# Optimization experiments

Measured on AMD Instinct MI355X. Metric: run time of the kernel, lower is better.

Reference implementation:

```python
import jax, jax.numpy as jnp
import numpy as np

B, S, D, H = 4, 1024, 1024, 16
DK = D // H
EPS = 1e-6

def setup_inputs() -> dict:
    key = jax.random.key(0)
    ks = jax.random.split(key, 7)
    scale = 1.0 / np.sqrt(D)
    return {
        "query": jax.random.normal(ks[0], (B, S, D), jnp.float32),
        "key": jax.random.normal(ks[1], (B, S, D), jnp.float32),
        "value": jax.random.normal(ks[2], (B, S, D), jnp.float32),
        "Wq": jax.random.normal(ks[3], (D, D), jnp.float32) * scale,
        "Wk": jax.random.normal(ks[4], (D, D), jnp.float32) * scale,
        "Wv": jax.random.normal(ks[5], (D, D), jnp.float32) * scale,
        "Wo": jax.random.normal(ks[6], (D, D), jnp.float32) * scale,
        "ln_gamma": jnp.ones((D,), jnp.float32),
        "ln_beta": jnp.zeros((D,), jnp.float32),
    }

def reference(query, key, value, Wq, Wk, Wv, Wo, ln_gamma, ln_beta):
    residual = query
    # projections (torch Linear: x @ W.T); reshape to [B,H,S,DK]
    def proj(x, W):
        y = jnp.einsum('bsd,ed->bse', x, W)
        return y.reshape(B, S, H, DK).transpose(0, 2, 1, 3)
    q, k, v = proj(query, Wq), proj(key, Wk), proj(value, Wv)
    scores = jnp.einsum('bhqd,bhkd->bhqk', q, k) / jnp.sqrt(jnp.float32(DK))
    p = jax.nn.softmax(scores, axis=-1)
    x = jnp.einsum('bhqk,bhkd->bhqd', p, v)
    x = x.transpose(0, 2, 1, 3).reshape(B, S, D)
    x = jnp.einsum('bsd,ed->bse', x, Wo)
    x = x + residual
    mu = jnp.mean(x, axis=-1, keepdims=True)
    var = jnp.var(x, axis=-1, keepdims=True)
    x = (x - mu) / jnp.sqrt(var + EPS) * ln_gamma + ln_beta
    return x
```

## Files before the change

kernel.cpp:

```cpp
#include <hip/hip_runtime.h>
#include <hip/hip_bf16.h>

#define B_ 4
#define S_ 1024
#define D_ 1024
#define H_ 16
#define DK_ 64
#define MROWS (B_*S_)

typedef short bf16x8 __attribute__((ext_vector_type(8)));
typedef float f32x4 __attribute__((ext_vector_type(4)));
typedef unsigned short u16;
typedef unsigned u32;
typedef u16 u16x4 __attribute__((ext_vector_type(4)));

__device__ __forceinline__ u16 f2bf(float f) {
    union { float f; unsigned u; } v; v.f = f;
    unsigned u = v.u;
    u += 0x7fff + ((u >> 16) & 1);
    return (u16)(u >> 16);
}

__device__ __forceinline__ void gld_lds16(const u16* gp, u16* lp) {
    __builtin_amdgcn_global_load_lds(
        (const __attribute__((address_space(1))) void*)gp,
        (__attribute__((address_space(3))) void*)lp,
        16, 0, 0);
}

__global__ __launch_bounds__(256) void pack_w(
    const float* __restrict__ wq, const float* __restrict__ wk,
    const float* __restrict__ wv, const float* __restrict__ wo,
    u16* __restrict__ w_dst)
{
    const int NW = 4 * D_ * D_;
    for (int c = blockIdx.x * blockDim.x + threadIdx.x;
         c < NW / 4; c += gridDim.x * blockDim.x) {
        int e = c * 4;
        int t = e >> 20;
        int off = e & (1048576 - 1);
        const float* s = (t == 0 ? wq : t == 1 ? wk : t == 2 ? wv : wo) + off;
        float4 tv = *(const float4*)s;
        u16x4 o; o[0]=f2bf(tv.x); o[1]=f2bf(tv.y); o[2]=f2bf(tv.z); o[3]=f2bf(tv.w);
        *(u16x4*)(w_dst + e) = o;
    }
}

__global__ __launch_bounds__(256) void gemm_qkv(
    const float* __restrict__ Aq, const float* __restrict__ Ak,
    const float* __restrict__ Avv, const u16* __restrict__ Wb,
    u16* __restrict__ Cb)
{
    __shared__ u16 ldsA[128 * 64];
    __shared__ u16 ldsB[128 * 64];

    const int gx = gridDim.x, gy = gridDim.y, gz = gridDim.z;
    const int nwg = gx * gy * gz;
    const int flat = blockIdx.x + gx * (blockIdx.y + gy * blockIdx.z);
    const int f = (flat & 7) * (nwg >> 3) + (flat >> 3);
    const int bx = f % gx;
    const int rem = f / gx;
    const int by = rem % gy;
    const int z = rem / gy;

    const float* Af = (z == 0) ? Aq : (z == 1) ? Ak : Avv;
    Wb += (size_t)z * D_ * D_;

    const int tid = threadIdx.x, lane = tid & 63, wid = tid >> 6;
    const int wr = wid >> 1, wc = wid & 1;
    const int m0 = by * 128, n0 = bx * 128;
    const int wbase = wid * 64;

    f32x4 acc[4][4] = {};

    for (int kt = 0; kt < 1024; kt += 64) {
        __syncthreads();
        #pragma unroll
        for (int j = 0; j < 4; ++j) {
            int g2 = j * 256 + tid;
            int row = g2 >> 3, c8 = g2 & 7;
            const float* src = Af + (size_t)(m0 + row) * 1024 + kt + c8 * 8;
            float4 a0 = *(const float4*)(src);
            float4 a1 = *(const float4*)(src + 4);
            bf16x8 o;
            o[0] = (short)f2bf(a0.x); o[1] = (short)f2bf(a0.y);
            o[2] = (short)f2bf(a0.z); o[3] = (short)f2bf(a0.w);
            o[4] = (short)f2bf(a1.x); o[5] = (short)f2bf(a1.y);
            o[6] = (short)f2bf(a1.z); o[7] = (short)f2bf(a1.w);
            int c8s = c8 ^ (row & 7);
            *(bf16x8*)(&ldsA[row * 64 + c8s * 8]) = o;
        }
        #pragma unroll
        for (int j = 0; j < 4; ++j) {
            int ch = j * 256 + tid;
            int row = ch >> 3, c8 = (ch & 7) ^ (row & 7);
            gld_lds16(Wb + (size_t)(n0 + row) * 1024 + kt + c8 * 8,
                      &ldsB[(j * 256 + wbase) * 8]);
        }
        __syncthreads();

        #pragma unroll
        for (int ks = 0; ks < 2; ++ks) {
            const int cb = ks * 32 + (lane >> 4) * 8;
            bf16x8 af[4], bfr[4];
            #pragma unroll
            for (int m = 0; m < 4; ++m) {
                int row = wr * 64 + m * 16 + (lane & 15);
                af[m] = *(const bf16x8*)(&ldsA[row * 64 + (cb ^ ((row & 7) << 3))]);
            }
            #pragma unroll
            for (int n = 0; n < 4; ++n) {
                int row = wc * 64 + n * 16 + (lane & 15);
                bfr[n] = *(const bf16x8*)(&ldsB[row * 64 + (cb ^ ((row & 7) << 3))]);
            }
            #pragma unroll
            for (int m = 0; m < 4; ++m)
                #pragma unroll
                for (int n = 0; n < 4; ++n)
                    acc[m][n] = __builtin_amdgcn_mfma_f32_16x16x32_bf16(
                        af[m], bfr[n], acc[m][n], 0, 0, 0);
        }
    }

    if (z == 2) {
        u16* Cz = Cb + 2 * (size_t)MROWS * D_;
        #pragma unroll
        for (int m = 0; m < 4; ++m)
            #pragma unroll
            for (int n = 0; n < 4; ++n) {
                u16x4 o;
                #pragma unroll
                for (int r = 0; r < 4; ++r) o[r] = f2bf(acc[m][n][r]);
                int grow = m0 + wr * 64 + m * 16 + (lane >> 4) * 4;
                int gcol = n0 + wc * 64 + n * 16 + (lane & 15);
                *(u16x4*)(&Cz[(size_t)gcol * MROWS + grow]) = o;
            }
    } else {
        u16* Cz = Cb + (size_t)z * MROWS * D_;
        #pragma unroll
        for (int m = 0; m < 4; ++m)
            #pragma unroll
            for (int n = 0; n < 4; ++n)
                #pragma unroll
                for (int r = 0; r < 4; ++r) {
                    int grow = m0 + wr * 64 + m * 16 + (lane >> 4) * 4 + r;
                    int gcol = n0 + wc * 64 + n * 16 + (lane & 15);
                    Cz[(size_t)grow * 1024 + gcol] = f2bf(acc[m][n][r]);
                }
    }
}

template<int BM, bool EPI_RESID, bool VT>
__global__ __launch_bounds__(256) void gemm_fast(
    const u16* __restrict__ Ab, const u16* __restrict__ Wb,
    u16* __restrict__ Cb, float* __restrict__ Cf, const float* __restrict__ resid)
{
    constexpr int WN = (BM == 128) ? 2 : 4;
    constexpr int WCOLS = 128 / WN;
    constexpr int NR = WCOLS / 16;
    __shared__ u16 ldsA[BM * 64];
    __shared__ u16 ldsB[128 * 64];

    const int gx = gridDim.x, gy = gridDim.y, gz = gridDim.z;
    const int nwg = gx * gy * gz;
    const int flat = blockIdx.x + gx * (blockIdx.y + gy * blockIdx.z);
    const int f = (flat & 7) * (nwg >> 3) + (flat >> 3);
    const int bx = f % gx;
    const int rem = f / gx;
    const int by = rem % gy;
    const int z = rem / gy;

    Ab += (size_t)z * MROWS * D_;
    Wb += (size_t)z * D_ * D_;
    const u16* CbT = Cb + (EPI_RESID ? 0 : (size_t)z * MROWS * D_);
    u16* Cbz = (u16*)CbT;

    const int tid = threadIdx.x, lane = tid & 63, wid = tid >> 6;
    const int wr = (BM == 128) ? (wid >> 1) : 0;
    const int wc = (BM == 128) ? (wid & 1) : wid;
    const int m0 = by * BM, n0 = bx * 128;
    const int wbase = wid * 64;

    f32x4 acc[4][NR] = {};

    for (int kt = 0; kt < 1024; kt += 64) {
        __syncthreads();
        #pragma unroll
        for (int j = 0; j < BM / 32; ++j) {
            int ch = j * 256 + tid;
            int row = ch >> 3, c8 = (ch & 7) ^ (row & 7);
            gld_lds16(Ab + (size_t)(m0 + row) * 1024 + kt + c8 * 8,
                      &ldsA[(j * 256 + wbase) * 8]);
        }
        #pragma unroll
        for (int j = 0; j < 4; ++j) {
            int ch = j * 256 + tid;
            int row = ch >> 3, c8 = (ch & 7) ^ (row & 7);
            gld_lds16(Wb + (size_t)(n0 + row) * 1024 + kt + c8 * 8,
                      &ldsB[(j * 256 + wbase) * 8]);
        }
        __syncthreads();

        #pragma unroll
        for (int ks = 0; ks < 2; ++ks) {
            const int cb = ks * 32 + (lane >> 4) * 8;
            bf16x8 af[4], bfr[NR];
            #pragma unroll
            for (int m = 0; m < 4; ++m) {
                int row = wr * 64 + m * 16 + (lane & 15);
                af[m] = *(const bf16x8*)(&ldsA[row * 64 + (cb ^ ((row & 7) << 3))]);
            }
            #pragma unroll
            for (int n = 0; n < NR; ++n) {
                int row = wc * WCOLS + n * 16 + (lane & 15);
                bfr[n] = *(const bf16x8*)(&ldsB[row * 64 + (cb ^ ((row & 7) << 3))]);
            }
            #pragma unroll
            for (int m = 0; m < 4; ++m)
                #pragma unroll
                for (int n = 0; n < NR; ++n)
                    acc[m][n] = __builtin_amdgcn_mfma_f32_16x16x32_bf16(
                        af[m], bfr[n], acc[m][n], 0, 0, 0);
        }
    }

    if (VT && z == 2) {
        #pragma unroll
        for (int m = 0; m < 4; ++m)
            #pragma unroll
            for (int n = 0; n < NR; ++n) {
                u16x4 o;
                #pragma unroll
                for (int r = 0; r < 4; ++r) o[r] = f2bf(acc[m][n][r]);
                int grow = m0 + wr * 64 + m * 16 + (lane >> 4) * 4;
                int gcol = n0 + wc * WCOLS + n * 16 + (lane & 15);
                *(u16x4*)(&Cbz[(size_t)gcol * MROWS + grow]) = o;
            }
    } else {
        #pragma unroll
        for (int m = 0; m < 4; ++m)
            #pragma unroll
            for (int n = 0; n < NR; ++n)
                #pragma unroll
                for (int r = 0; r < 4; ++r) {
                    int grow = m0 + wr * 64 + m * 16 + (lane >> 4) * 4 + r;
                    int gcol = n0 + wc * WCOLS + n * 16 + (lane & 15);
                    if (EPI_RESID)
                        Cf[(size_t)grow * 1024 + gcol] = acc[m][n][r] + resid[(size_t)grow * 1024 + gcol];
                    else
                        Cbz[(size_t)grow * 1024 + gcol] = f2bf(acc[m][n][r]);
                }
    }
}

template<bool A_BF16, bool EPI_RESID>
__global__ __launch_bounds__(256) void gemm_bt(
    const void* __restrict__ Av, const float* __restrict__ Bw,
    u16* __restrict__ Cb, float* __restrict__ Cf,
    const float* __restrict__ resid, int M, int N, int K)
{
    __shared__ u16 lds[2][128 * 64];
    const int tid  = threadIdx.x;
    const int lane = tid & 63;
    const int wid  = tid >> 6;
    const int wr = wid >> 1, wc = wid & 1;
    const int m0 = blockIdx.y * 128, n0 = blockIdx.x * 128;

    f32x4 acc[4][4] = {};

    for (int kt = 0; kt < K; kt += 64) {
        #pragma unroll
        for (int j = 0; j < 8; ++j) {
            int idx4 = tid + 256 * j;
            int r = idx4 >> 4;
            int c = (idx4 & 15) * 4;
            u16x4 aw, bw;
            if (A_BF16) {
                const u16* Ab2 = (const u16*)Av;
                aw = *(const u16x4*)(Ab2 + (size_t)(m0 + r) * K + kt + c);
            } else {
                const float* Af = (const float*)Av;
                float4 t = *(const float4*)(Af + (size_t)(m0 + r) * K + kt + c);
                aw[0] = f2bf(t.x); aw[1] = f2bf(t.y); aw[2] = f2bf(t.z); aw[3] = f2bf(t.w);
            }
            {
                float4 t = *(const float4*)(Bw + (size_t)(n0 + r) * K + kt + c);
                bw[0] = f2bf(t.x); bw[1] = f2bf(t.y); bw[2] = f2bf(t.z); bw[3] = f2bf(t.w);
            }
            int sa = r * 64 + (c ^ ((r & 7) << 3));
            *(u16x4*)(&lds[0][sa]) = aw;
            *(u16x4*)(&lds[1][sa]) = bw;
        }
        __syncthreads();
        #pragma unroll
        for (int ks = 0; ks < 2; ++ks) {
            const int cb = ks * 32 + (lane >> 4) * 8;
            bf16x8 af[4], bfr[4];
            #pragma unroll
            for (int m = 0; m < 4; ++m) {
                int row = wr * 64 + m * 16 + (lane & 15);
                af[m] = *(const bf16x8*)(&lds[0][row * 64 + (cb ^ ((row & 7) << 3))]);
            }
            #pragma unroll
            for (int n = 0; n < 4; ++n) {
                int row = wc * 64 + n * 16 + (lane & 15);
                bfr[n] = *(const bf16x8*)(&lds[1][row * 64 + (cb ^ ((row & 7) << 3))]);
            }
            #pragma unroll
            for (int m = 0; m < 4; ++m)
                #pragma unroll
                for (int n = 0; n < 4; ++n)
                    acc[m][n] = __builtin_amdgcn_mfma_f32_16x16x32_bf16(
                        af[m], bfr[n], acc[m][n], 0, 0, 0);
        }
        __syncthreads();
    }

    #pragma unroll
    for (int m = 0; m < 4; ++m)
        #pragma unroll
        for (int n = 0; n < 4; ++n)
            #pragma unroll
            for (int r = 0; r < 4; ++r) {
                int grow = m0 + wr * 64 + m * 16 + (lane >> 4) * 4 + r;
                int gcol = n0 + wc * 64 + n * 16 + (lane & 15);
                float v = acc[m][n][r];
                if (EPI_RESID)
                    Cf[(size_t)grow * N + gcol] = v + resid[(size_t)grow * N + gcol];
                else
                    Cb[(size_t)grow * N + gcol] = f2bf(v);
            }
}

__global__ __launch_bounds__(512, 4) void attn_fwd5(
    const u16* __restrict__ Qg, const u16* __restrict__ Kg,
    const u16* __restrict__ Vt, u16* __restrict__ Og)
{
    __shared__ u16 qs[128 * 64];
    __shared__ u16 ks2[64 * 64];
    __shared__ u16 vsT[64 * 64];
    __shared__ u16 ps[128 * 64];

    const int tid = threadIdx.x, lane = tid & 63, w = tid >> 6;
    const int g = lane >> 4, ql = lane & 15;

    const int bid = blockIdx.x;
    const int f = (bid & 7) * 64 + (bid >> 3);
    const int qt = f & 7, h = (f >> 3) & 15, b = f >> 7;
    const int q0 = qt * 128;
    const size_t rbase = (size_t)b * S_;
    const int cb0 = h * DK_;

    auto stage_kv = [&](int kv0) {
        {
            int ch = tid;
            int row = ch >> 3, c8 = (ch & 7) ^ (row & 7);
            gld_lds16(Kg + (rbase + kv0 + row) * D_ + cb0 + c8 * 8, &ks2[w * 512]);
        }
        {
            int ch = tid;
            int row = ch >> 3, c8 = (ch & 7) ^ (row & 7);
            gld_lds16(Vt + (size_t)(cb0 + row) * MROWS + rbase + kv0 + c8 * 8, &vsT[w * 512]);
        }
    };

    #pragma unroll
    for (int j = 0; j < 2; ++j) {
        int idx = j * 512 + tid;
        int row = idx >> 3, c8 = (idx & 7) ^ (row & 7);
        gld_lds16(Qg + (rbase + q0 + row) * D_ + cb0 + c8 * 8,
                  &qs[(j * 512 + w * 64) * 8]);
    }
    stage_kv(0);
    __syncthreads();

    bf16x8 qb[2];
    {
        const int q = w * 16 + ql;
        #pragma unroll
        for (int ks = 0; ks < 2; ++ks) {
            int c = 32 * ks + 8 * g;
            qb[ks] = *(const bf16x8*)(&qs[q * 64 + (c ^ ((q & 7) << 3))]);
        }
    }

    float mrow = -1e30f, lrow = 0.f;
    f32x4 xacc[4] = {};

    for (int jt = 0; jt < 16; ++jt) {
        f32x4 sacc[4] = {};
        __builtin_amdgcn_s_setprio(1);
        #pragma unroll
        for (int ks = 0; ks < 2; ++ks) {
            #pragma unroll
            for (int n = 0; n < 4; ++n) {
                int krow = n * 16 + ql;
                int c = 32 * ks + 8 * g;
                bf16x8 kf = *(const bf16x8*)(&ks2[krow * 64 + (c ^ ((krow & 7) << 3))]);
                sacc[n] = __builtin_amdgcn_mfma_f32_16x16x32_bf16(kf, qb[ks], sacc[n], 0, 0, 0);
            }
        }
        __builtin_amdgcn_s_setprio(0);

        float mt = sacc[0][0];
        #pragma unroll
        for (int n = 0; n < 4; ++n)
            #pragma unroll
            for (int r = 0; r < 4; ++r) mt = fmaxf(mt, sacc[n][r]);
        mt = fmaxf(mt, __shfl_xor(mt, 16));
        mt = fmaxf(mt, __shfl_xor(mt, 32));
        float mnew = fmaxf(mrow, mt * 0.125f);
        float alpha = __expf(mrow - mnew);
        float rsum = 0.f;
        u16 pb[16];
        #pragma unroll
        for (int n = 0; n < 4; ++n)
            #pragma unroll
            for (int r = 0; r < 4; ++r) {
                float p = __expf(sacc[n][r] * 0.125f - mnew);
                rsum += p;
                pb[n * 4 + r] = f2bf(p);
            }
        rsum += __shfl_xor(rsum, 16);
        rsum += __shfl_xor(rsum, 32);
        lrow = lrow * alpha + rsum;
        mrow = mnew;

        {
            const int q = w * 16 + ql;
            #pragma unroll
            for (int n = 0; n < 4; ++n) {
                int c = 16 * n + 4 * g;
                *(u16x4*)(&ps[q * 64 + (c ^ ((q & 7) << 3))]) = *(const u16x4*)(&pb[n * 4]);
            }
        }
        asm volatile("s_waitcnt lgkmcnt(0)" ::: "memory");
        __builtin_amdgcn_sched_barrier(0);

        bf16x8 pa[2];
        {
            const int q = w * 16 + ql;
            #pragma unroll
            for (int ks = 0; ks < 2; ++ks) {
                int c = 32 * ks + 8 * g;
                pa[ks] = *(const bf16x8*)(&ps[q * 64 + (c ^ ((q & 7) << 3))]);
            }
        }
        #pragma unroll
        for (int r = 0; r < 4; ++r) {
            float a_r = __shfl(alpha, 4 * g + r);
            #pragma unroll
            for (int n2 = 0; n2 < 4; ++n2) xacc[n2][r] *= a_r;
        }

        __builtin_amdgcn_s_setprio(1);
        #pragma unroll
        for (int ks = 0; ks < 2; ++ks)
            #pragma unroll
            for (int n2 = 0; n2 < 4; ++n2) {
                int vrow = n2 * 16 + ql;
                int c2 = 32 * ks + 8 * g;
                bf16x8 bv = *(const bf16x8*)(&vsT[vrow * 64 + (c2 ^ ((vrow & 7) << 3))]);
                xacc[n2] = __builtin_amdgcn_mfma_f32_16x16x32_bf16(pa[ks], bv, xacc[n2], 0, 0, 0);
            }
        __builtin_amdgcn_s_setprio(0);

        if (jt < 15) {
            __syncthreads();
            stage_kv((jt + 1) * 64);
            __syncthreads();
        }
    }

    float linv[4];
    #pragma unroll
    for (int r = 0; r < 4; ++r) linv[r] = 1.f / __shfl(lrow, 4 * g + r);
    #pragma unroll
    for (int n2 = 0; n2 < 4; ++n2)
        #pragma unroll
        for (int r = 0; r < 4; ++r) {
            int qrow = q0 + w * 16 + 4 * g + r;
            int col = cb0 + n2 * 16 + ql;
            Og[(rbase + qrow) * D_ + col] = f2bf(xacc[n2][r] * linv[r]);
        }
}

__global__ __launch_bounds__(256) void attn_fwd(
    const u16* __restrict__ Qg, const u16* __restrict__ Kg,
    const u16* __restrict__ Vg, u16* __restrict__ Og)
{
    __shared__ u16 qs[64 * 64], ks2[64 * 64], vt[64 * 64], ps[64 * 64];
    const int tid = threadIdx.x, lane = tid & 63, w = tid >> 6;
    const int b = blockIdx.z, h = blockIdx.y, q0 = blockIdx.x * 64;
    const size_t rbase = (size_t)b * S_;
    const int cb0 = h * DK_;

    #pragma unroll
    for (int j = 0; j < 4; ++j) {
        int idx4 = tid + 256 * j;
        int r = idx4 >> 4, c = (idx4 & 15) * 4;
        u16x4 t = *(const u16x4*)(Qg + (rbase + q0 + r) * D_ + cb0 + c);
        *(u16x4*)(&qs[r * 64 + (c ^ ((r & 7) << 3))]) = t;
    }

    float mrow[4], lrow[4];
    f32x4 xacc[4] = {};
    #pragma unroll
    for (int r = 0; r < 4; ++r) { mrow[r] = -1e30f; lrow[r] = 0.f; }

    for (int jt = 0; jt < 16; ++jt) {
        const int kv0 = jt * 64;
        __syncthreads();
        #pragma unroll
        for (int j = 0; j < 4; ++j) {
            int idx4 = tid + 256 * j;
            int r = idx4 >> 4, c = (idx4 & 15) * 4;
            u16x4 t = *(const u16x4*)(Kg + (rbase + kv0 + r) * D_ + cb0 + c);
            *(u16x4*)(&ks2[r * 64 + (c ^ ((r & 7) << 3))]) = t;
            u16x4 tv = *(const u16x4*)(Vg + (rbase + kv0 + r) * D_ + cb0 + c);
            #pragma unroll
            for (int jj = 0; jj < 4; ++jj) {
                int d = c + jj;
                vt[d * 64 + (r ^ ((d & 7) << 3))] = tv[jj];
            }
        }
        __syncthreads();

        f32x4 sacc[4] = {};
        #pragma unroll
        for (int ks = 0; ks < 2; ++ks) {
            const int cb = ks * 32 + (lane >> 4) * 8;
            int qrow = w * 16 + (lane & 15);
            bf16x8 aq = *(const bf16x8*)(&qs[qrow * 64 + (cb ^ ((qrow & 7) << 3))]);
            #pragma unroll
            for (int n = 0; n < 4; ++n) {
                int krow = n * 16 + (lane & 15);
                bf16x8 bk = *(const bf16x8*)(&ks2[krow * 64 + (cb ^ ((krow & 7) << 3))]);
                sacc[n] = __builtin_amdgcn_mfma_f32_16x16x32_bf16(aq, bk, sacc[n], 0, 0, 0);
            }
        }

        #pragma unroll
        for (int r = 0; r < 4; ++r) {
            float mx = fmaxf(fmaxf(sacc[0][r], sacc[1][r]),
                             fmaxf(sacc[2][r], sacc[3][r]));
            mx = fmaxf(mx, __shfl_xor(mx, 1));
            mx = fmaxf(mx, __shfl_xor(mx, 2));
            mx = fmaxf(mx, __shfl_xor(mx, 4));
            mx = fmaxf(mx, __shfl_xor(mx, 8));
            float mnew = fmaxf(mrow[r], mx * 0.125f);
            float alpha = __expf(mrow[r] - mnew);
            float p[4], rsum = 0.f;
            #pragma unroll
            for (int n = 0; n < 4; ++n) { p[n] = __expf(sacc[n][r] * 0.125f - mnew); rsum += p[n]; }
            rsum += __shfl_xor(rsum, 1);
            rsum += __shfl_xor(rsum, 2);
            rsum += __shfl_xor(rsum, 4);
            rsum += __shfl_xor(rsum, 8);
            lrow[r] = lrow[r] * alpha + rsum;
            mrow[r] = mnew;
            int qrow = w * 16 + (lane >> 4) * 4 + r;
            #pragma unroll
            for (int n = 0; n < 4; ++n) {
                xacc[n][r] *= alpha;
                int col = n * 16 + (lane & 15);
                ps[qrow * 64 + (col ^ ((qrow & 7) << 3))] = f2bf(p[n]);
            }
        }
        __syncthreads();

        #pragma unroll
        for (int ks = 0; ks < 2; ++ks) {
            const int cb = ks * 32 + (lane >> 4) * 8;
            int prow = w * 16 + (lane & 15);
            bf16x8 ap = *(const bf16x8*)(&ps[prow * 64 + (cb ^ ((prow & 7) << 3))]);
            #pragma unroll
            for (int n = 0; n < 4; ++n) {
                int vrow = n * 16 + (lane & 15);
                bf16x8 bv = *(const bf16x8*)(&vt[vrow * 64 + (cb ^ ((vrow & 7) << 3))]);
                xacc[n] = __builtin_amdgcn_mfma_f32_16x16x32_bf16(ap, bv, xacc[n], 0, 0, 0);
            }
        }
    }

    #pragma unroll
    for (int n = 0; n < 4; ++n)
        #pragma unroll
        for (int r = 0; r < 4; ++r) {
            int qrow = q0 + w * 16 + (lane >> 4) * 4 + r;
            int col = cb0 + n * 16 + (lane & 15);
            Og[(rbase + qrow) * D_ + col] = f2bf(xacc[n][r] / lrow[r]);
        }
}

__global__ __launch_bounds__(256) void ln_inplace(
    float* __restrict__ Y, const float* __restrict__ g, const float* __restrict__ bt)
{
    __shared__ float red[2][4];
    const int row = blockIdx.x, tid = threadIdx.x;
    float4 v = *(const float4*)(Y + (size_t)row * D_ + tid * 4);
    float s = v.x + v.y + v.z + v.w;
    float q = v.x * v.x + v.y * v.y + v.z * v.z + v.w * v.w;
    #pragma unroll
    for (int m = 1; m < 64; m <<= 1) { s += __shfl_xor(s, m); q += __shfl_xor(q, m); }
    const int w = tid >> 6, lane = tid & 63;
    if (lane == 0) { red[0][w] = s; red[1][w] = q; }
    __syncthreads();
    s = red[0][0] + red[0][1] + red[0][2] + red[0][3];
    q = red[1][0] + red[1][1] + red[1][2] + red[1][3];
    float mu = s * (1.f / 1024.f);
    float var = q * (1.f / 1024.f) - mu * mu;
    float rstd = rsqrtf(var + 1e-6f);
    float4 gv = *(const float4*)(g + tid * 4);
    float4 bv = *(const float4*)(bt + tid * 4);
    v.x = (v.x - mu) * rstd * gv.x + bv.x;
    v.y = (v.y - mu) * rstd * gv.y + bv.y;
    v.z = (v.z - mu) * rstd * gv.z + bv.z;
    v.w = (v.w - mu) * rstd * gv.w + bv.w;
    *(float4*)(Y + (size_t)row * D_ + tid * 4) = v;
}

extern "C" void kernel_launch(void* const* d_in, const int* in_sizes, int n_in,
                              void* d_out, int out_size, void* d_ws, size_t ws_size,
                              hipStream_t stream)
{
    const float* query = (const float*)d_in[0];
    const float* key   = (const float*)d_in[1];
    const float* value = (const float*)d_in[2];
    const float* Wq    = (const float*)d_in[3];
    const float* Wk    = (const float*)d_in[4];
    const float* Wv    = (const float*)d_in[5];
    const float* Wo    = (const float*)d_in[6];
    const float* gamma = (const float*)d_in[7];
    const float* beta  = (const float*)d_in[8];
    float* out = (float*)d_out;

    const size_t ACT = (size_t)MROWS * D_;
    const size_t WSZ = (size_t)D_ * D_;
    const size_t NEED = (4 * WSZ + 4 * ACT) * 2;

    if (ws_size >= NEED) {
        u16* wb = (u16*)d_ws;
        u16* pb = wb + 4 * WSZ;
        u16* Ap = pb + 3 * ACT;

        pack_w<<<1024, 256, 0, stream>>>(Wq, Wk, Wv, Wo, wb);
        gemm_qkv<<<dim3(8, 32, 3), 256, 0, stream>>>(query, key, value, wb, pb);
        attn_fwd5<<<512, 512, 0, stream>>>(pb, pb + ACT, pb + 2 * ACT, Ap);
        gemm_fast<64, true, false><<<dim3(8, 64, 1), 256, 0, stream>>>(Ap, wb + 3 * WSZ, nullptr, out, query);
        ln_inplace<<<MROWS, 256, 0, stream>>>(out, gamma, beta);
    } else {
        u16* Qp = (u16*)d_ws;
        u16* Kp = Qp + ACT;
        u16* Vp = Kp + ACT;
        u16* Ap = Vp + ACT;
        dim3 gg(D_ / 128, MROWS / 128);
        gemm_bt<false, false><<<gg, 256, 0, stream>>>(query, Wq, Qp, nullptr, nullptr, MROWS, D_, D_);
        gemm_bt<false, false><<<gg, 256, 0, stream>>>(key,   Wk, Kp, nullptr, nullptr, MROWS, D_, D_);
        gemm_bt<false, false><<<gg, 256, 0, stream>>>(value, Wv, Vp, nullptr, nullptr, MROWS, D_, D_);
        attn_fwd<<<dim3(S_ / 64, H_, B_), 256, 0, stream>>>(Qp, Kp, Vp, Ap);
        gemm_bt<true, true><<<gg, 256, 0, stream>>>(Ap, Wo, nullptr, out, query, MROWS, D_, D_);
        ln_inplace<<<MROWS, 256, 0, stream>>>(out, gamma, beta);
    }
}
```

Baseline: 127.0 us.

## Pre-convert activations to bf16 and use 256x128 async-loaded QKV GEMM tiles

The fp32 query/key/value activations are now converted to bf16 in the packing kernel along with the weights. The QKV projection then loads both operands straight into LDS with global_load_lds, instead of doing fp32 loads and converting in registers inside the GEMM loop. The GEMM tile grows to 256x128 with 512 threads. This adds an extra pass that writes and rereads 24MB of bf16 activations, in exchange for a leaner GEMM inner loop and better operand reuse. The attention output buffer now aliases the activation staging area.

```diff
diff --git a/kernel.cpp b/kernel.cpp
--- a/kernel.cpp
+++ b/kernel.cpp
@@ -28,34 +28,45 @@
         16, 0, 0);
 }
 
-__global__ __launch_bounds__(256) void pack_w(
+__global__ __launch_bounds__(256) void pack_bf16(
+    const float* __restrict__ q, const float* __restrict__ k, const float* __restrict__ v,
     const float* __restrict__ wq, const float* __restrict__ wk,
     const float* __restrict__ wv, const float* __restrict__ wo,
-    u16* __restrict__ w_dst)
-{
-    const int NW = 4 * D_ * D_;
+    u16* __restrict__ act_dst, u16* __restrict__ w_dst)
+{
+    const int NACT = 3 * MROWS * D_;
+    const int NW   = 4 * D_ * D_;
     for (int c = blockIdx.x * blockDim.x + threadIdx.x;
-         c < NW / 4; c += gridDim.x * blockDim.x) {
+         c < (NACT + NW) / 4; c += gridDim.x * blockDim.x) {
         int e = c * 4;
-        int t = e >> 20;
-        int off = e & (1048576 - 1);
-        const float* s = (t == 0 ? wq : t == 1 ? wk : t == 2 ? wv : wo) + off;
+        const float* s; u16* d;
+        if (e < NACT) {
+            int t = e >> 22;
+            int off = e & (4194304 - 1);
+            s = (t == 0 ? q : t == 1 ? k : v) + off;
+            d = act_dst + e;
+        } else {
+            int e2 = e - NACT;
+            int t = e2 >> 20;
+            int off = e2 & (1048576 - 1);
+            s = (t == 0 ? wq : t == 1 ? wk : t == 2 ? wv : wo) + off;
+            d = w_dst + e2;
+        }
         float4 tv = *(const float4*)s;
         u16x4 o; o[0]=f2bf(tv.x); o[1]=f2bf(tv.y); o[2]=f2bf(tv.z); o[3]=f2bf(tv.w);
-        *(u16x4*)(w_dst + e) = o;
-    }
-}
-
-__global__ __launch_bounds__(256) void gemm_qkv(
-    const float* __restrict__ Aq, const float* __restrict__ Ak,
-    const float* __restrict__ Avv, const u16* __restrict__ Wb,
+        *(u16x4*)d = o;
+    }
+}
+
+__global__ __launch_bounds__(512) void gemm_qkv2(
+    const u16* __restrict__ Ab, const u16* __restrict__ Wb,
     u16* __restrict__ Cb)
 {
-    __shared__ u16 ldsA[128 * 64];
+    __shared__ u16 ldsA[256 * 64];
     __shared__ u16 ldsB[128 * 64];
 
-    const int gx = gridDim.x, gy = gridDim.y, gz = gridDim.z;
-    const int nwg = gx * gy * gz;
+    const int gx = gridDim.x, gy = gridDim.y;
+    const int nwg = gx * gy * gridDim.z;
     const int flat = blockIdx.x + gx * (blockIdx.y + gy * blockIdx.z);
     const int f = (flat & 7) * (nwg >> 3) + (flat >> 3);
     const int bx = f % gx;
@@ -63,12 +74,13 @@
     const int by = rem % gy;
     const int z = rem / gy;
 
-    const float* Af = (z == 0) ? Aq : (z == 1) ? Ak : Avv;
+    Ab += (size_t)z * MROWS * D_;
     Wb += (size_t)z * D_ * D_;
 
     const int tid = threadIdx.x, lane = tid & 63, wid = tid >> 6;
     const int wr = wid >> 1, wc = wid & 1;
-    const int m0 = by * 128, n0 = bx * 128;
+    const int ql = lane & 15;
+    const int m0 = by * 256, n0 = bx * 128;
     const int wbase = wid * 64;
 
     f32x4 acc[4][4] = {};
@@ -77,25 +89,17 @@
         __syncthreads();
         #pragma unroll
         for (int j = 0; j < 4; ++j) {
-            int g2 = j * 256 + tid;
-            int row = g2 >> 3, c8 = g2 & 7;
-            const float* src = Af + (size_t)(m0 + row) * 1024 + kt + c8 * 8;
-            float4 a0 = *(const float4*)(src);
-            float4 a1 = *(const float4*)(src + 4);
-            bf16x8 o;
-            o[0] = (short)f2bf(a0.x); o[1] = (short)f2bf(a0.y);
-            o[2] = (short)f2bf(a0.z); o[3] = (short)f2bf(a0.w);
-            o[4] = (short)f2bf(a1.x); o[5] = (short)f2bf(a1.y);
-            o[6] = (short)f2bf(a1.z); o[7] = (short)f2bf(a1.w);
-            int c8s = c8 ^ (row & 7);
-            *(bf16x8*)(&ldsA[row * 64 + c8s * 8]) = o;
-        }
-        #pragma unroll
-        for (int j = 0; j < 4; ++j) {
-            int ch = j * 256 + tid;
+            int ch = j * 512 + tid;
+            int row = ch >> 3, c8 = (ch & 7) ^ (row & 7);
+            gld_lds16(Ab + (size_t)(m0 + row) * 1024 + kt + c8 * 8,
+                      &ldsA[(j * 512 + wbase) * 8]);
+        }
+        #pragma unroll
+        for (int j = 0; j < 2; ++j) {
+            int ch = j * 512 + tid;
             int row = ch >> 3, c8 = (ch & 7) ^ (row & 7);
             gld_lds16(Wb + (size_t)(n0 + row) * 1024 + kt + c8 * 8,
-                      &ldsB[(j * 256 + wbase) * 8]);
+                      &ldsB[(j * 512 + wbase) * 8]);
         }
         __syncthreads();
 
@@ -105,12 +109,12 @@
             bf16x8 af[4], bfr[4];
             #pragma unroll
             for (int m = 0; m < 4; ++m) {
-                int row = wr * 64 + m * 16 + (lane & 15);
+                int row = wr * 64 + m * 16 + ql;
                 af[m] = *(const bf16x8*)(&ldsA[row * 64 + (cb ^ ((row & 7) << 3))]);
             }
             #pragma unroll
             for (int n = 0; n < 4; ++n) {
-                int row = wc * 64 + n * 16 + (lane & 15);
+                int row = wc * 64 + n * 16 + ql;
                 bfr[n] = *(const bf16x8*)(&ldsB[row * 64 + (cb ^ ((row & 7) << 3))]);
             }
             #pragma unroll
@@ -132,7 +136,7 @@
                 #pragma unroll
                 for (int r = 0; r < 4; ++r) o[r] = f2bf(acc[m][n][r]);
                 int grow = m0 + wr * 64 + m * 16 + (lane >> 4) * 4;
-                int gcol = n0 + wc * 64 + n * 16 + (lane & 15);
+                int gcol = n0 + wc * 64 + n * 16 + ql;
                 *(u16x4*)(&Cz[(size_t)gcol * MROWS + grow]) = o;
             }
     } else {
@@ -144,7 +148,7 @@
                 #pragma unroll
                 for (int r = 0; r < 4; ++r) {
                     int grow = m0 + wr * 64 + m * 16 + (lane >> 4) * 4 + r;
-                    int gcol = n0 + wc * 64 + n * 16 + (lane & 15);
+                    int gcol = n0 + wc * 64 + n * 16 + ql;
                     Cz[(size_t)grow * 1024 + gcol] = f2bf(acc[m][n][r]);
                 }
     }
@@ -637,15 +641,16 @@
 
     const size_t ACT = (size_t)MROWS * D_;
     const size_t WSZ = (size_t)D_ * D_;
-    const size_t NEED = (4 * WSZ + 4 * ACT) * 2;
+    const size_t NEED = (3 * ACT + 4 * WSZ + 3 * ACT) * 2;
 
     if (ws_size >= NEED) {
-        u16* wb = (u16*)d_ws;
-        u16* pb = wb + 4 * WSZ;
-        u16* Ap = pb + 3 * ACT;
-
-        pack_w<<<1024, 256, 0, stream>>>(Wq, Wk, Wv, Wo, wb);
-        gemm_qkv<<<dim3(8, 32, 3), 256, 0, stream>>>(query, key, value, wb, pb);
+        u16* actb = (u16*)d_ws;
+        u16* wb   = actb + 3 * ACT;
+        u16* pb   = wb + 4 * WSZ;
+        u16* Ap   = actb;
+
+        pack_bf16<<<2048, 256, 0, stream>>>(query, key, value, Wq, Wk, Wv, Wo, actb, wb);
+        gemm_qkv2<<<dim3(8, 16, 3), 512, 0, stream>>>(actb, wb, pb);
         attn_fwd5<<<512, 512, 0, stream>>>(pb, pb + ACT, pb + 2 * ACT, Ap);
         gemm_fast<64, true, false><<<dim3(8, 64, 1), 256, 0, stream>>>(Ap, wb + 3 * WSZ, nullptr, out, query);
         ln_inplace<<<MROWS, 256, 0, stream>>>(out, gamma, beta);
```

New measurement: 131.3 us. +3.4%, slower.
